# Performance work log

Measured on AMD Instinct MI355X. Metric: run time of the kernel, lower is better.

Reference implementation:

```python
import jax, jax.numpy as jnp
import numpy as np

B, S, HID = 2, 2048, 3072
NH, NKV, HD = 24, 8, 128  # num_heads, kv heads, head_dim
G = NH // NKV             # GQA group size = 3
SCALING = HD ** -0.5
LAYER_SCALING = 1.0       # sqrt(layer_number=1)


def setup_inputs() -> dict:
    key = jax.random.key(0)
    ks = jax.random.split(key, 10)
    std = 0.02
    inp = {
        "hidden_states": jax.random.normal(ks[0], (B, S, HID), jnp.float32),
        # additive causal mask: 0 on/below diag, -1e9 above
        "attention_mask": jnp.where(
            jnp.tril(jnp.ones((S, S), bool)), 0.0, -1e9
        ).astype(jnp.float32)[None, None],
        # torch nn.Linear layout: W is [out, in]
        "Wq": jax.random.normal(ks[1], (HID, HID), jnp.float32) * std,
        "bq": jnp.zeros((HID,), jnp.float32),
        "Wk": jax.random.normal(ks[2], (NKV * HD, HID), jnp.float32) * std,
        "bk": jnp.zeros((NKV * HD,), jnp.float32),
        "Wv": jax.random.normal(ks[3], (NKV * HD, HID), jnp.float32) * std,
        "bv": jnp.zeros((NKV * HD,), jnp.float32),
        "Wd": jax.random.normal(ks[4], (HID, HID), jnp.float32) * std,
        "bd": jnp.zeros((HID,), jnp.float32),
    }
    return inp


def reference(hidden_states, attention_mask, Wq, bq, Wk, bk, Wv, bv, Wd, bd):
    b, s, _ = hidden_states.shape
    q = hidden_states @ Wq.T + bq                     # [B,S,HID]
    k = hidden_states @ Wk.T + bk                     # [B,S,NKV*HD]
    v = hidden_states @ Wv.T + bv
    # grouped layout: q [B,NKV,G,S,D]; repeat_interleave(dim=1) == grouped kv head
    q = q.reshape(b, s, NKV, G, HD).transpose(0, 2, 3, 1, 4)
    k = k.reshape(b, s, NKV, HD).transpose(0, 2, 1, 3)  # [B,NKV,S,D]
    v = v.reshape(b, s, NKV, HD).transpose(0, 2, 1, 3)
    scores = jnp.einsum("bhgqd,bhkd->bhgqk", q, k)
    scores = scores * (SCALING / LAYER_SCALING)
    scores = scores + attention_mask[:, :, None]       # broadcast over kv-head/group
    probs = jax.nn.softmax(scores.astype(jnp.float32), axis=-1).astype(scores.dtype)
    ctx = jnp.einsum("bhgqk,bhkd->bhgqd", probs, v)    # [B,NKV,G,S,D]
    # (kv_head, group) flattened == repeat_interleave head ordering
    ctx = ctx.transpose(0, 3, 1, 2, 4).reshape(b, s, HID)
    return ctx @ Wd.T + bd
```

## Files before the change

kernel.cpp:

```cpp
#include <hip/hip_runtime.h>

typedef unsigned short ushort_t;
typedef unsigned int uint32;
typedef __bf16 bf16x8 __attribute__((ext_vector_type(8)));
typedef float f32x4 __attribute__((ext_vector_type(4)));

#define MFMA16(a, b, c) __builtin_amdgcn_mfma_f32_16x16x32_bf16((a), (b), (c), 0, 0, 0)

__device__ __forceinline__ ushort_t f2bf(float f) {
  union { float f; uint32 u; } c; c.f = f;
  uint32 u = c.u;
  u += 0x7fffu + ((u >> 16) & 1u);
  return (ushort_t)(u >> 16);
}

__device__ __forceinline__ void gload_lds16(const void* g, void* l) {
  __builtin_amdgcn_global_load_lds(
      (const __attribute__((address_space(1))) void*)g,
      (__attribute__((address_space(3))) void*)l, 16, 0, 0);
}

__global__ __launch_bounds__(256)
void cvt5_kernel(const float* __restrict__ p0, const float* __restrict__ p1,
                 const float* __restrict__ p2, const float* __restrict__ p3,
                 const float* __restrict__ p4, ushort_t* __restrict__ out) {
  const size_t B0 = 12582912;
  const size_t B1 = B0 + 9437184;
  const size_t B2 = B1 + 3145728;
  const size_t B3 = B2 + 3145728;
  const size_t B4 = B3 + 9437184;
  const size_t step = (size_t)gridDim.x * 256 * 4;
  for (size_t g = ((size_t)blockIdx.x * 256 + threadIdx.x) * 4; g < B4; g += step) {
    const float* src; size_t off;
    if (g < B0)      { src = p0; off = 0;  }
    else if (g < B1) { src = p1; off = B0; }
    else if (g < B2) { src = p2; off = B1; }
    else if (g < B3) { src = p3; off = B2; }
    else             { src = p4; off = B3; }
    float4 v = *(const float4*)(src + (g - off));
    union { uint2 u; ushort_t s[4]; } p;
    p.s[0] = f2bf(v.x); p.s[1] = f2bf(v.y);
    p.s[2] = f2bf(v.z); p.s[3] = f2bf(v.w);
    *(uint2*)(out + g) = p.u;
  }
}

#define GEMM_BODY(ABASE, WROWBASE, KD)                                          \
  f32x4 acc[4][4] = {};                                                         \
  const int nk = (KD) >> 6;                                                     \
  for (int kt = 0; kt < nk; ++kt) {                                             \
    _Pragma("unroll")                                                           \
    for (int i = 0; i < 4; ++i) {                                               \
      int o = (i * 256 + tid) * 16;                                             \
      int row = o >> 7;                                                         \
      int src = (o & 127) ^ ((row & 7) << 4);                                   \
      gload_lds16(ABASE + (rowA0 + row) * (KD) + kt * 64 + (src >> 1),          \
                  (char*)As + o);                                               \
      gload_lds16(WROWBASE + (size_t)row * (KD) + kt * 64 + (src >> 1),         \
                  (char*)Bs + o);                                               \
    }                                                                           \
    __syncthreads();                                                            \
    bf16x8 af[4][2], bfr[4][2];                                                 \
    _Pragma("unroll")                                                           \
    for (int mi = 0; mi < 4; ++mi) {                                            \
      int row = wr * 64 + mi * 16 + l15;                                        \
      _Pragma("unroll")                                                         \
      for (int kk = 0; kk < 2; ++kk) {                                          \
        int boff = (row * 128 + kk * 64 + lg * 16) ^ ((row & 7) << 4);          \
        af[mi][kk] = *(const bf16x8*)((const char*)As + boff);                  \
      }                                                                         \
    }                                                                           \
    _Pragma("unroll")                                                           \
    for (int nj = 0; nj < 4; ++nj) {                                            \
      int row = wc * 64 + nj * 16 + l15;                                        \
      _Pragma("unroll")                                                         \
      for (int kk = 0; kk < 2; ++kk) {                                          \
        int boff = (row * 128 + kk * 64 + lg * 16) ^ ((row & 7) << 4);          \
        bfr[nj][kk] = *(const bf16x8*)((const char*)Bs + boff);                 \
      }                                                                         \
    }                                                                           \
    _Pragma("unroll")                                                           \
    for (int mi = 0; mi < 4; ++mi)                                              \
      _Pragma("unroll")                                                         \
      for (int nj = 0; nj < 4; ++nj)                                            \
        _Pragma("unroll")                                                       \
        for (int kk = 0; kk < 2; ++kk)                                          \
          acc[mi][nj] = MFMA16(af[mi][kk], bfr[nj][kk], acc[mi][nj]);           \
    __syncthreads();                                                            \
  }

__global__ __launch_bounds__(256)
void qkv_gemm_kernel(const ushort_t* __restrict__ A,
                     const ushort_t* __restrict__ Wq, const ushort_t* __restrict__ Wk,
                     const ushort_t* __restrict__ Wv,
                     const float* __restrict__ bq, const float* __restrict__ bk,
                     const float* __restrict__ bv, ushort_t* __restrict__ C)
{
  __shared__ __attribute__((aligned(16))) ushort_t As[128 * 64];
  __shared__ __attribute__((aligned(16))) ushort_t Bs[128 * 64];
  const int tid = threadIdx.x;
  const int lane = tid & 63;
  const int wv_ = tid >> 6;
  const int wr = wv_ >> 1, wc = wv_ & 1;
  const int x = blockIdx.x & 7;
  const int li = blockIdx.x >> 3;
  const int bm = ((x & 1) << 4) | (li & 15);
  const int bn = (x >> 1) * 10 + (li >> 4);
  const int l15 = lane & 15, lg = lane >> 4;

  const ushort_t* Wsrc; const float* bsrc; int nloc;
  if (bn < 24)      { Wsrc = Wq; bsrc = bq; nloc = bn << 7; }
  else if (bn < 32) { Wsrc = Wk; bsrc = bk; nloc = (bn - 24) << 7; }
  else              { Wsrc = Wv; bsrc = bv; nloc = (bn - 32) << 7; }

  const size_t rowA0 = (size_t)bm * 128;
  const ushort_t* Wrow = Wsrc + (size_t)nloc * 3072;

  GEMM_BODY(A, Wrow, 3072)

#pragma unroll
  for (int nj = 0; nj < 4; ++nj) {
    int cl = wc * 64 + nj * 16 + l15;
    float bvl = bsrc[nloc + cl];
    int col = bn * 128 + cl;
#pragma unroll
    for (int mi = 0; mi < 4; ++mi) {
      int row0 = bm * 128 + wr * 64 + mi * 16 + lg * 4;
#pragma unroll
      for (int r = 0; r < 4; ++r)
        C[(size_t)(row0 + r) * 5120 + col] = f2bf(acc[mi][nj][r] + bvl);
    }
  }
}

template <bool OUT_F32>
__global__ __launch_bounds__(256)
void gemm_bt_kernel(const ushort_t* __restrict__ A, const ushort_t* __restrict__ W,
                    const float* __restrict__ bias, void* __restrict__ Cv,
                    int N, int Kd, int cbn)
{
  __shared__ __attribute__((aligned(16))) ushort_t As[128 * 64];
  __shared__ __attribute__((aligned(16))) ushort_t Bs[128 * 64];
  const int tid = threadIdx.x;
  const int lane = tid & 63;
  const int wv_ = tid >> 6;
  const int wr = wv_ >> 1, wc = wv_ & 1;
  const int x = blockIdx.x & 7;
  const int li = blockIdx.x >> 3;
  const int bm = ((x & 1) << 4) | (li & 15);
  const int bn = (x >> 1) * cbn + (li >> 4);
  const int l15 = lane & 15, lg = lane >> 4;

  const size_t rowA0 = (size_t)bm * 128;
  const ushort_t* Wrow = W + (size_t)(bn * 128) * Kd;

  GEMM_BODY(A, Wrow, Kd)

#pragma unroll
  for (int nj = 0; nj < 4; ++nj) {
    int col = bn * 128 + wc * 64 + nj * 16 + l15;
    float bvl = bias[col];
#pragma unroll
    for (int mi = 0; mi < 4; ++mi) {
      int row0 = bm * 128 + wr * 64 + mi * 16 + lg * 4;
#pragma unroll
      for (int r = 0; r < 4; ++r) {
        float v = acc[mi][nj][r] + bvl;
        if (OUT_F32) ((float*)Cv)[(size_t)(row0 + r) * N + col] = v;
        else         ((ushort_t*)Cv)[(size_t)(row0 + r) * N + col] = f2bf(v);
      }
    }
  }
}

#define NHEADS 24
#define GRP 3
#define SEQ 2048
#define QSCL 0.12751745f
#define DTHR 8.0f

__global__ __launch_bounds__(256)
void attn_kernel(const ushort_t* __restrict__ QKV, ushort_t* __restrict__ O)
{
  __shared__ __attribute__((aligned(16))) ushort_t Kl[2][64 * 128];
  __shared__ __attribute__((aligned(16))) ushort_t Vt[128 * 64];

  const int tid = threadIdx.x;
  const int lane = tid & 63;
  const int wv = tid >> 6;
  const int l15 = lane & 15, lg = lane >> 4;
  const int bh = blockIdx.x;
  const int qb = 31 - blockIdx.y;
  const int b = bh / NHEADS, h = bh % NHEADS;
  const int kvh = h / GRP;
  const size_t kbase = (size_t)b * SEQ * 5120 + 3072 + (size_t)kvh * 128;
  const size_t vbase = kbase + 1024;
  const int q0 = qb * 64;

  const int kv4 = (tid & 15) * 4;
  const int d8 = (tid >> 4) * 8;
  const int a_sel = lg >> 1;
  const int s0l = (lane & 15) + 32 * (lg & 1);

#pragma unroll
  for (int i = 0; i < 4; ++i) {
    int o = (i * 256 + tid) * 16;
    int row = o >> 8;
    int src = (o & 255) ^ ((row & 7) << 4);
    gload_lds16(QKV + kbase + (size_t)row * 5120 + (src >> 1), (char*)&Kl[0][0] + o);
  }
  uint4 vr0, vr1, vr2, vr3;
  {
    const ushort_t* vg = QKV + vbase + (size_t)kv4 * 5120 + d8;
    vr0 = *(const uint4*)(vg);
    vr1 = *(const uint4*)(vg + 5120);
    vr2 = *(const uint4*)(vg + 10240);
    vr3 = *(const uint4*)(vg + 15360);
  }

  bf16x8 qf[4];
  {
    const ushort_t* qg = QKV + (size_t)(b * SEQ + q0 + wv * 16 + l15) * 5120 + h * 128 + lg * 8;
#pragma unroll
    for (int c = 0; c < 4; ++c) {
      bf16x8 q = *(const bf16x8*)(qg + c * 32);
#pragma unroll
      for (int e = 0; e < 8; ++e) q[e] = (__bf16)((float)q[e] * QSCL);
      qf[c] = q;
    }
  }

  float m_st = -1e30f, l_st = 0.f;
  f32x4 accO[8] = {};

  for (int t = 0; t <= qb; ++t) {
    const int cur = t & 1;
    {
      union { uint4 u; ushort_t s[8]; } L0, L1, L2, L3;
      L0.u = vr0; L1.u = vr1; L2.u = vr2; L3.u = vr3;
#pragma unroll
      for (int dd = 0; dd < 8; ++dd) {
        int d = d8 + dd;
        uint2 w;
        w.x = (uint32)L0.s[dd] | ((uint32)L1.s[dd] << 16);
        w.y = (uint32)L2.s[dd] | ((uint32)L3.s[dd] << 16);
        int swz = ((d & 7) ^ ((d >> 3) & 3)) << 4;
        int off = (d * 128 + kv4 * 2) ^ swz;
        *(uint2*)((char*)Vt + off) = w;
      }
    }
    asm volatile("s_waitcnt lgkmcnt(0)" ::: "memory");
    __builtin_amdgcn_s_barrier();

    if (t < qb) {
      const int kvn = (t + 1) * 64;
#pragma unroll
      for (int i = 0; i < 4; ++i) {
        int o = (i * 256 + tid) * 16;
        int row = o >> 8;
        int src = (o & 255) ^ ((row & 7) << 4);
        gload_lds16(QKV + kbase + (size_t)(kvn + row) * 5120 + (src >> 1),
                    (char*)&Kl[cur ^ 1][0] + o);
      }
      const ushort_t* vg = QKV + vbase + (size_t)(kvn + kv4) * 5120 + d8;
      vr0 = *(const uint4*)(vg);
      vr1 = *(const uint4*)(vg + 5120);
      vr2 = *(const uint4*)(vg + 10240);
      vr3 = *(const uint4*)(vg + 15360);
    }

    f32x4 s[4];
    __builtin_amdgcn_s_setprio(1);
#pragma unroll
    for (int n = 0; n < 4; ++n) {
      f32x4 z = {0.f, 0.f, 0.f, 0.f};
      s[n] = z;
#pragma unroll
      for (int c = 0; c < 4; ++c) {
        int row = n * 16 + l15;
        int boff = (row * 256 + c * 64 + lg * 16) ^ ((row & 7) << 4);
        bf16x8 kf = *(const bf16x8*)((const char*)Kl[cur] + boff);
        s[n] = MFMA16(kf, qf[c], s[n]);
      }
    }
    __builtin_amdgcn_s_setprio(0);

    if (t == qb) {
      const int qg_ = wv * 16 + l15;
#pragma unroll
      for (int n = 0; n < 4; ++n)
#pragma unroll
        for (int r = 0; r < 4; ++r)
          if (n * 16 + lg * 4 + r > qg_) s[n][r] = -1e9f;
    }

    float mx = fmaxf(fmaxf(fmaxf(s[0][0], s[0][1]), fmaxf(s[0][2], s[0][3])),
                     fmaxf(fmaxf(s[1][0], s[1][1]), fmaxf(s[1][2], s[1][3])));
    mx = fmaxf(mx, fmaxf(fmaxf(fmaxf(s[2][0], s[2][1]), fmaxf(s[2][2], s[2][3])),
                         fmaxf(fmaxf(s[3][0], s[3][1]), fmaxf(s[3][2], s[3][3]))));
    mx = fmaxf(mx, __shfl_xor(mx, 16, 64));
    mx = fmaxf(mx, __shfl_xor(mx, 32, 64));

    if (!__all(mx <= m_st + DTHR)) {
      const float mnew = fmaxf(m_st, mx);
      const float alpha = __builtin_amdgcn_exp2f(m_st - mnew);
      m_st = mnew;
      l_st *= alpha;
#pragma unroll
      for (int j = 0; j < 8; ++j)
#pragma unroll
        for (int r = 0; r < 4; ++r) accO[j][r] *= alpha;
    }

    float rsum = 0.f;
    uint32 dwA[4], dwB[4];
#pragma unroll
    for (int n = 0; n < 4; ++n) {
      float p0 = __builtin_amdgcn_exp2f(s[n][0] - m_st);
      float p1 = __builtin_amdgcn_exp2f(s[n][1] - m_st);
      float p2 = __builtin_amdgcn_exp2f(s[n][2] - m_st);
      float p3 = __builtin_amdgcn_exp2f(s[n][3] - m_st);
      rsum += (p0 + p1) + (p2 + p3);
      dwA[n] = (uint32)f2bf(p0) | ((uint32)f2bf(p1) << 16);
      dwB[n] = (uint32)f2bf(p2) | ((uint32)f2bf(p3) << 16);
    }
    rsum += __shfl_xor(rsum, 16, 64);
    rsum += __shfl_xor(rsum, 32, 64);
    l_st += rsum;

#pragma unroll
    for (int c = 0; c < 2; ++c) {
      uint32 xA0 = __shfl((int)dwA[2 * c],     s0l,      64);
      uint32 xB0 = __shfl((int)dwB[2 * c],     s0l,      64);
      uint32 xA1 = __shfl((int)dwA[2 * c + 1], s0l,      64);
      uint32 xB1 = __shfl((int)dwB[2 * c + 1], s0l,      64);
      uint32 yA0 = __shfl((int)dwA[2 * c],     s0l + 16, 64);
      uint32 yB0 = __shfl((int)dwB[2 * c],     s0l + 16, 64);
      uint32 yA1 = __shfl((int)dwA[2 * c + 1], s0l + 16, 64);
      uint32 yB1 = __shfl((int)dwB[2 * c + 1], s0l + 16, 64);
      union { uint4 u; bf16x8 v; } pb;
      pb.u.x = a_sel ? xA1 : xA0;
      pb.u.y = a_sel ? xB1 : xB0;
      pb.u.z = a_sel ? yA1 : yA0;
      pb.u.w = a_sel ? yB1 : yB0;
      __builtin_amdgcn_s_setprio(1);
#pragma unroll
      for (int j = 0; j < 8; ++j) {
        int d = j * 16 + l15;
        int swz = ((d & 7) ^ ((d >> 3) & 3)) << 4;
        int off = (d * 128 + c * 64 + lg * 16) ^ swz;
        bf16x8 vf = *(const bf16x8*)((const char*)Vt + off);
        accO[j] = MFMA16(vf, pb.v, accO[j]);
      }
      __builtin_amdgcn_s_setprio(0);
    }
    __builtin_amdgcn_s_barrier();
  }

  const float inv = 1.0f / l_st;
  ushort_t* og = O + (size_t)(b * SEQ + q0 + wv * 16 + l15) * 3072 + h * 128 + lg * 4;
#pragma unroll
  for (int j = 0; j < 8; ++j) {
    union { uint2 u; ushort_t s[4]; } w;
    w.s[0] = f2bf(accO[j][0] * inv);
    w.s[1] = f2bf(accO[j][1] * inv);
    w.s[2] = f2bf(accO[j][2] * inv);
    w.s[3] = f2bf(accO[j][3] * inv);
    *(uint2*)(og + j * 16) = w.u;
  }
}

extern "C" void kernel_launch(void* const* d_in, const int* in_sizes, int n_in,
                              void* d_out, int out_size, void* d_ws, size_t ws_size,
                              hipStream_t stream) {
  const float* hs = (const float*)d_in[0];
  const float* Wq = (const float*)d_in[2];
  const float* bq = (const float*)d_in[3];
  const float* Wk = (const float*)d_in[4];
  const float* bk = (const float*)d_in[5];
  const float* Wv = (const float*)d_in[6];
  const float* bv = (const float*)d_in[7];
  const float* Wd = (const float*)d_in[8];
  const float* bd = (const float*)d_in[9];
  float* out = (float*)d_out;

  const size_t N_HS = (size_t)4096 * 3072;
  const size_t N_WQ = (size_t)3072 * 3072;
  const size_t N_WK = (size_t)1024 * 3072;

  ushort_t* hs_bf = (ushort_t*)d_ws;
  ushort_t* Wq_bf = hs_bf + N_HS;
  ushort_t* Wk_bf = Wq_bf + N_WQ;
  ushort_t* Wv_bf = Wk_bf + N_WK;
  ushort_t* Wd_bf = Wv_bf + N_WK;
  ushort_t* QKVw  = Wd_bf + N_WQ;
  ushort_t* Cw    = hs_bf;

  dim3 blk(256);
  cvt5_kernel<<<2048, blk, 0, stream>>>(hs, Wq, Wk, Wv, Wd, hs_bf);
  qkv_gemm_kernel<<<dim3(1280), blk, 0, stream>>>(hs_bf, Wq_bf, Wk_bf, Wv_bf,
                                                  bq, bk, bv, QKVw);
  attn_kernel<<<dim3(48, 32), blk, 0, stream>>>(QKVw, Cw);
  gemm_bt_kernel<true><<<dim3(24 * 32), blk, 0, stream>>>(Cw, Wd_bf, bd, out, 3072, 3072, 6);
}
```

Baseline: 452.5 us.

## Rewrite projection GEMMs with 256x256 tiles, 8 waves, 4-stage async LDS pipeline

Replaces the two 128x128, 4-wave, single-buffered GEMM kernels with one templated 512-thread kernel. It computes 256x256 output tiles using a K-step of 32, a 4-deep ring of LDS buffers filled by global_load_lds, and vmcnt-based waits instead of two barriers per step. It also raises wave priority around the MFMA bursts. The aim is to hide global-load latency and get more reuse per tile, in exchange for more LDS, more accumulator registers and fewer blocks (320 and 192) on the GPU.

```diff
diff --git a/kernel.cpp b/kernel.cpp
--- a/kernel.cpp
+++ b/kernel.cpp
@@ -45,129 +45,126 @@
   }
 }
 
-#define GEMM_BODY(ABASE, WROWBASE, KD)                                          \
-  f32x4 acc[4][4] = {};                                                         \
-  const int nk = (KD) >> 6;                                                     \
-  for (int kt = 0; kt < nk; ++kt) {                                             \
-    _Pragma("unroll")                                                           \
-    for (int i = 0; i < 4; ++i) {                                               \
-      int o = (i * 256 + tid) * 16;                                             \
-      int row = o >> 7;                                                         \
-      int src = (o & 127) ^ ((row & 7) << 4);                                   \
-      gload_lds16(ABASE + (rowA0 + row) * (KD) + kt * 64 + (src >> 1),          \
-                  (char*)As + o);                                               \
-      gload_lds16(WROWBASE + (size_t)row * (KD) + kt * 64 + (src >> 1),         \
-                  (char*)Bs + o);                                               \
-    }                                                                           \
-    __syncthreads();                                                            \
-    bf16x8 af[4][2], bfr[4][2];                                                 \
-    _Pragma("unroll")                                                           \
-    for (int mi = 0; mi < 4; ++mi) {                                            \
-      int row = wr * 64 + mi * 16 + l15;                                        \
-      _Pragma("unroll")                                                         \
-      for (int kk = 0; kk < 2; ++kk) {                                          \
-        int boff = (row * 128 + kk * 64 + lg * 16) ^ ((row & 7) << 4);          \
-        af[mi][kk] = *(const bf16x8*)((const char*)As + boff);                  \
-      }                                                                         \
-    }                                                                           \
-    _Pragma("unroll")                                                           \
-    for (int nj = 0; nj < 4; ++nj) {                                            \
-      int row = wc * 64 + nj * 16 + l15;                                        \
-      _Pragma("unroll")                                                         \
-      for (int kk = 0; kk < 2; ++kk) {                                          \
-        int boff = (row * 128 + kk * 64 + lg * 16) ^ ((row & 7) << 4);          \
-        bfr[nj][kk] = *(const bf16x8*)((const char*)Bs + boff);                 \
-      }                                                                         \
-    }                                                                           \
-    _Pragma("unroll")                                                           \
-    for (int mi = 0; mi < 4; ++mi)                                              \
-      _Pragma("unroll")                                                         \
-      for (int nj = 0; nj < 4; ++nj)                                            \
-        _Pragma("unroll")                                                       \
-        for (int kk = 0; kk < 2; ++kk)                                          \
-          acc[mi][nj] = MFMA16(af[mi][kk], bfr[nj][kk], acc[mi][nj]);           \
-    __syncthreads();                                                            \
-  }
-
-__global__ __launch_bounds__(256)
-void qkv_gemm_kernel(const ushort_t* __restrict__ A,
-                     const ushort_t* __restrict__ Wq, const ushort_t* __restrict__ Wk,
-                     const ushort_t* __restrict__ Wv,
-                     const float* __restrict__ bq, const float* __restrict__ bk,
-                     const float* __restrict__ bv, ushort_t* __restrict__ C)
+template <bool IS_QKV, bool OUT_F32>
+__global__ __launch_bounds__(512)
+void gemm8p_kernel(const ushort_t* __restrict__ A,
+                   const ushort_t* __restrict__ W0, const ushort_t* __restrict__ W1,
+                   const ushort_t* __restrict__ W2,
+                   const float* __restrict__ b0, const float* __restrict__ b1,
+                   const float* __restrict__ b2,
+                   void* __restrict__ Cv, int ldc, int Kd)
 {
-  __shared__ __attribute__((aligned(16))) ushort_t As[128 * 64];
-  __shared__ __attribute__((aligned(16))) ushort_t Bs[128 * 64];
+  __shared__ __attribute__((aligned(16))) char As[4][16384];
+  __shared__ __attribute__((aligned(16))) char Bs[4][16384];
+
   const int tid = threadIdx.x;
   const int lane = tid & 63;
-  const int wv_ = tid >> 6;
-  const int wr = wv_ >> 1, wc = wv_ & 1;
+  const int wid = tid >> 6;
+  const int wr = wid >> 2;
+  const int wc = wid & 3;
+  const int l15 = lane & 15, lg = lane >> 4;
+
   const int x = blockIdx.x & 7;
   const int li = blockIdx.x >> 3;
-  const int bm = ((x & 1) << 4) | (li & 15);
-  const int bn = (x >> 1) * 10 + (li >> 4);
-  const int l15 = lane & 15, lg = lane >> 4;
-
-  const ushort_t* Wsrc; const float* bsrc; int nloc;
-  if (bn < 24)      { Wsrc = Wq; bsrc = bq; nloc = bn << 7; }
-  else if (bn < 32) { Wsrc = Wk; bsrc = bk; nloc = (bn - 24) << 7; }
-  else              { Wsrc = Wv; bsrc = bv; nloc = (bn - 32) << 7; }
-
-  const size_t rowA0 = (size_t)bm * 128;
-  const ushort_t* Wrow = Wsrc + (size_t)nloc * 3072;
-
-  GEMM_BODY(A, Wrow, 3072)
+  const int bm = (x << 1) | (li & 1);
+  const int bn = li >> 1;
+
+  const ushort_t* Wseg; const float* bseg; int nloc;
+  if constexpr (IS_QKV) {
+    if (bn < 12)      { Wseg = W0; bseg = b0; nloc = bn << 8; }
+    else if (bn < 16) { Wseg = W1; bseg = b1; nloc = (bn - 12) << 8; }
+    else              { Wseg = W2; bseg = b2; nloc = (bn - 16) << 8; }
+  } else { Wseg = W0; bseg = b0; nloc = bn << 8; }
+
+  const size_t rowA0 = (size_t)bm * 256;
+  const int nt = Kd >> 5;
+
+  auto stage = [&](int kt, int buf) {
+#pragma unroll
+    for (int i = 0; i < 2; ++i) {
+      int o = (i * 512 + tid) * 16;
+      int R = o >> 7;
+      int sg = ((o >> 4) & 7) ^ (R & 7);
+      int grow = 2 * R + (sg >> 2);
+      int gk = (sg & 3) * 8;
+      gload_lds16(A + (rowA0 + grow) * Kd + kt * 32 + gk, &As[buf][o]);
+    }
+#pragma unroll
+    for (int i = 0; i < 2; ++i) {
+      int o = (i * 512 + tid) * 16;
+      int R = o >> 7;
+      int sg = ((o >> 4) & 7) ^ (R & 7);
+      int grow = 2 * R + (sg >> 2);
+      int gk = (sg & 3) * 8;
+      gload_lds16(Wseg + (size_t)(nloc + grow) * Kd + kt * 32 + gk, &Bs[buf][o]);
+    }
+  };
+
+  f32x4 acc[8][4] = {};
+
+  stage(0, 0); stage(1, 1); stage(2, 2);
+
+  for (int t = 0; t < nt; ++t) {
+    const int buf = t & 3;
+    const int ahead = nt - 1 - t;
+    if (ahead >= 2)      asm volatile("s_waitcnt vmcnt(8)" ::: "memory");
+    else if (ahead == 1) asm volatile("s_waitcnt vmcnt(4)" ::: "memory");
+    else                 asm volatile("s_waitcnt vmcnt(0)" ::: "memory");
+    __builtin_amdgcn_s_barrier();
+    if (t + 3 < nt) stage(t + 3, (t + 3) & 3);
+
+    bf16x8 bfr[4];
+#pragma unroll
+    for (int nj = 0; nj < 4; ++nj) {
+      int br = wc * 64 + nj * 16 + l15;
+      int R = br >> 1;
+      int off = R * 128 + (((((br & 1) << 2) | lg) ^ (R & 7)) << 4);
+      bfr[nj] = *(const bf16x8*)(&Bs[buf][off]);
+    }
+    bf16x8 af[4];
+#pragma unroll
+    for (int mi = 0; mi < 4; ++mi) {
+      int ar = wr * 128 + mi * 16 + l15;
+      int R = ar >> 1;
+      int off = R * 128 + (((((ar & 1) << 2) | lg) ^ (R & 7)) << 4);
+      af[mi] = *(const bf16x8*)(&As[buf][off]);
+    }
+    __builtin_amdgcn_s_setprio(1);
+#pragma unroll
+    for (int mi = 0; mi < 4; ++mi)
+#pragma unroll
+      for (int nj = 0; nj < 4; ++nj)
+        acc[mi][nj] = MFMA16(af[mi], bfr[nj], acc[mi][nj]);
+    __builtin_amdgcn_s_setprio(0);
+#pragma unroll
+    for (int mi = 0; mi < 4; ++mi) {
+      int ar = wr * 128 + 64 + mi * 16 + l15;
+      int R = ar >> 1;
+      int off = R * 128 + (((((ar & 1) << 2) | lg) ^ (R & 7)) << 4);
+      af[mi] = *(const bf16x8*)(&As[buf][off]);
+    }
+    __builtin_amdgcn_s_setprio(1);
+#pragma unroll
+    for (int mi = 0; mi < 4; ++mi)
+#pragma unroll
+      for (int nj = 0; nj < 4; ++nj)
+        acc[4 + mi][nj] = MFMA16(af[mi], bfr[nj], acc[4 + mi][nj]);
+    __builtin_amdgcn_s_setprio(0);
+  }
 
 #pragma unroll
   for (int nj = 0; nj < 4; ++nj) {
     int cl = wc * 64 + nj * 16 + l15;
-    float bvl = bsrc[nloc + cl];
-    int col = bn * 128 + cl;
-#pragma unroll
-    for (int mi = 0; mi < 4; ++mi) {
-      int row0 = bm * 128 + wr * 64 + mi * 16 + lg * 4;
-#pragma unroll
-      for (int r = 0; r < 4; ++r)
-        C[(size_t)(row0 + r) * 5120 + col] = f2bf(acc[mi][nj][r] + bvl);
-    }
-  }
-}
-
-template <bool OUT_F32>
-__global__ __launch_bounds__(256)
-void gemm_bt_kernel(const ushort_t* __restrict__ A, const ushort_t* __restrict__ W,
-                    const float* __restrict__ bias, void* __restrict__ Cv,
-                    int N, int Kd, int cbn)
-{
-  __shared__ __attribute__((aligned(16))) ushort_t As[128 * 64];
-  __shared__ __attribute__((aligned(16))) ushort_t Bs[128 * 64];
-  const int tid = threadIdx.x;
-  const int lane = tid & 63;
-  const int wv_ = tid >> 6;
-  const int wr = wv_ >> 1, wc = wv_ & 1;
-  const int x = blockIdx.x & 7;
-  const int li = blockIdx.x >> 3;
-  const int bm = ((x & 1) << 4) | (li & 15);
-  const int bn = (x >> 1) * cbn + (li >> 4);
-  const int l15 = lane & 15, lg = lane >> 4;
-
-  const size_t rowA0 = (size_t)bm * 128;
-  const ushort_t* Wrow = W + (size_t)(bn * 128) * Kd;
-
-  GEMM_BODY(A, Wrow, Kd)
-
-#pragma unroll
-  for (int nj = 0; nj < 4; ++nj) {
-    int col = bn * 128 + wc * 64 + nj * 16 + l15;
-    float bvl = bias[col];
-#pragma unroll
-    for (int mi = 0; mi < 4; ++mi) {
-      int row0 = bm * 128 + wr * 64 + mi * 16 + lg * 4;
+    float bvl = bseg[nloc + cl];
+    int col = bn * 256 + cl;
+#pragma unroll
+    for (int mi = 0; mi < 8; ++mi) {
+      int row0 = bm * 256 + wr * 128 + mi * 16 + lg * 4;
 #pragma unroll
       for (int r = 0; r < 4; ++r) {
         float v = acc[mi][nj][r] + bvl;
-        if (OUT_F32) ((float*)Cv)[(size_t)(row0 + r) * N + col] = v;
-        else         ((ushort_t*)Cv)[(size_t)(row0 + r) * N + col] = f2bf(v);
+        if (OUT_F32) ((float*)Cv)[(size_t)(row0 + r) * ldc + col] = v;
+        else         ((ushort_t*)Cv)[(size_t)(row0 + r) * ldc + col] = f2bf(v);
       }
     }
   }
@@ -396,10 +393,10 @@
   ushort_t* QKVw  = Wd_bf + N_WQ;
   ushort_t* Cw    = hs_bf;
 
-  dim3 blk(256);
-  cvt5_kernel<<<2048, blk, 0, stream>>>(hs, Wq, Wk, Wv, Wd, hs_bf);
-  qkv_gemm_kernel<<<dim3(1280), blk, 0, stream>>>(hs_bf, Wq_bf, Wk_bf, Wv_bf,
-                                                  bq, bk, bv, QKVw);
-  attn_kernel<<<dim3(48, 32), blk, 0, stream>>>(QKVw, Cw);
-  gemm_bt_kernel<true><<<dim3(24 * 32), blk, 0, stream>>>(Cw, Wd_bf, bd, out, 3072, 3072, 6);
-}
+  cvt5_kernel<<<dim3(2048), dim3(256), 0, stream>>>(hs, Wq, Wk, Wv, Wd, hs_bf);
+  gemm8p_kernel<true, false><<<dim3(320), dim3(512), 0, stream>>>(
+      hs_bf, Wq_bf, Wk_bf, Wv_bf, bq, bk, bv, QKVw, 5120, 3072);
+  attn_kernel<<<dim3(48, 32), dim3(256), 0, stream>>>(QKVw, Cw);
+  gemm8p_kernel<false, true><<<dim3(192), dim3(512), 0, stream>>>(
+      Cw, Wd_bf, nullptr, nullptr, bd, nullptr, nullptr, out, 3072, 3072);
+}
```

Result: slower. 526.5 us (+16.4%).
